# Kernel optimization log

Hardware: AMD Instinct MI355X
Metric: run time of the kernel (lower is better)

Reference implementation:

```python
import jax, jax.numpy as jnp
import numpy as np

F_DIM = 128
RBF_DIM = 20
N_NODES = 10000
N_EDGES = 200000
CUTOFF = 5


def setup_inputs() -> dict:
    key = jax.random.key(0)
    ks = jax.random.split(key, 12)
    s = jax.random.normal(ks[0], (N_NODES, F_DIM), jnp.float32)
    vec = jax.random.normal(ks[1], (N_NODES, 3, F_DIM), jnp.float32)
    edge_indexes = jax.random.randint(ks[2], (2, N_EDGES), 0, N_NODES, jnp.int32)
    edge_vector = jax.random.normal(ks[3], (N_EDGES, 3), jnp.float32)
    # distances in (0.5, 5.0) so fcut is nontrivial and no divide-by-zero
    edge_distance = jax.random.uniform(ks[4], (N_EDGES,), jnp.float32) * 4.5 + 0.5
    edge_rbf = jax.random.normal(ks[5], (N_EDGES, RBF_DIM), jnp.float32)
    # params: linear_s = Linear(F,F) -> SiLU -> Linear(F,3F); linear_rbf = Linear(RBF,3F)
    Ws1 = jax.random.normal(ks[6], (F_DIM, F_DIM), jnp.float32) / np.sqrt(F_DIM)
    bs1 = jnp.zeros((F_DIM,), jnp.float32)
    Ws2 = jax.random.normal(ks[7], (3 * F_DIM, F_DIM), jnp.float32) / np.sqrt(F_DIM)
    bs2 = jnp.zeros((3 * F_DIM,), jnp.float32)
    Wrbf = jax.random.normal(ks[8], (3 * F_DIM, RBF_DIM), jnp.float32) / np.sqrt(RBF_DIM)
    brbf = jnp.zeros((3 * F_DIM,), jnp.float32)
    return {
        "s": s, "vec": vec, "edge_vector": edge_vector,
        "edge_distance": edge_distance, "edge_rbf": edge_rbf,
        "Ws1": Ws1, "bs1": bs1, "Ws2": Ws2, "bs2": bs2,
        "Wrbf": Wrbf, "brbf": brbf,
        "edge_indexes": edge_indexes, "cutoff_dist": CUTOFF,
    }


def reference(s, vec, edge_vector, edge_distance, edge_rbf,
              Ws1, bs1, Ws2, bs2, Wrbf, brbf,
              edge_indexes, cutoff_dist):
    num_atoms, nf = s.shape
    dst_recv = edge_indexes[0]   # index_add target (message receivers)
    src_send = edge_indexes[1]   # gather source (message senders)

    S = s[src_send]              # [E, F]
    Vec = vec[src_send]          # [E, 3, F]

    # linear_s: Linear -> SiLU -> Linear
    h = jax.nn.silu(S @ Ws1.T + bs1)          # [E, F]
    phi = h @ Ws2.T + bs2                      # [E, 3F]

    rbf_lin = edge_rbf @ Wrbf.T + brbf         # [E, 3F]
    # cosine cutoff: 0.5*(cos(pi*d/rc)+1) for d < rc else 0
    rc = jnp.asarray(cutoff_dist, edge_distance.dtype)
    fcut = 0.5 * (jnp.cos(jnp.pi * edge_distance / rc) + 1.0)
    fcut = jnp.where(edge_distance < rc, fcut, 0.0)

    W = rbf_lin * fcut[:, None]
    vec_Ws, vec_Wvv, vec_Wvs = jnp.split(phi * W, 3, axis=-1)  # each [E, F]

    ds = jnp.zeros((num_atoms, nf), s.dtype).at[dst_recv].add(vec_Ws)

    vec_n = edge_vector / edge_distance[:, None]               # [E, 3]
    dVec = vec_Wvv[:, None, :] * Vec + vec_n[:, :, None] * vec_Wvs[:, None, :]  # [E,3,F]
    dvec = jnp.zeros((num_atoms, 3, nf), s.dtype).at[dst_recv].add(dVec)

    return ds, dvec
```

## Files before the change

### kernel.cpp

```cpp
#include <hip/hip_runtime.h>
#include <hip/hip_bf16.h>

typedef __attribute__((ext_vector_type(8))) short short8;
typedef __attribute__((ext_vector_type(4))) float floatx4;
typedef _Float16 half2_t __attribute__((ext_vector_type(2)));

#define CAP 64

__device__ __forceinline__ unsigned short f2bf(float x) {
    unsigned u = __float_as_uint(x);
    unsigned r = u + 0x7fffu + ((u >> 16) & 1u);
    return (unsigned short)(r >> 16);
}
__device__ __forceinline__ float bf2f(unsigned short h) {
    return __uint_as_float(((unsigned)h) << 16);
}
__device__ __forceinline__ unsigned short f2h(float x) {
    _Float16 h = (_Float16)x;
    return __builtin_bit_cast(unsigned short, h);
}
__device__ __forceinline__ float FD(unsigned int a, unsigned int b, float c) {
#if __has_builtin(__builtin_amdgcn_fdot2)
    return __builtin_amdgcn_fdot2(__builtin_bit_cast(half2_t, a),
                                  __builtin_bit_cast(half2_t, b), c, false);
#else
    half2_t ha = __builtin_bit_cast(half2_t, a);
    half2_t hb = __builtin_bit_cast(half2_t, b);
    return c + (float)ha[0] * (float)hb[0] + (float)ha[1] * (float)hb[1];
#endif
}
__device__ __forceinline__ float decode_rc(const void* cutoff_raw) {
    float fv = ((const float*)cutoff_raw)[0];
    int   iv = ((const int*)cutoff_raw)[0];
    if (fv > 0.099f && fv < 1.0e6f) return fv;
    if (iv > 0 && iv < 1000000) return (float)iv;
    double dv = ((const double*)cutoff_raw)[0];
    if (dv > 0.099 && dv < 1.0e6) return (float)dv;
    return (float)(((const long long*)cutoff_raw)[0]);
}

__global__ void setup_kernel(const float* __restrict__ vec,
                             const float* __restrict__ Ws1,
                             const float* __restrict__ Ws2,
                             const float* __restrict__ Wrbf,
                             const float* __restrict__ edge_rbf,
                             const int* __restrict__ eidx,
                             const float* __restrict__ edge_vec,
                             const float* __restrict__ edge_dist,
                             const void* __restrict__ cutoff_raw,
                             unsigned short* __restrict__ P6,
                             unsigned short* __restrict__ ws1_bf,
                             unsigned short* __restrict__ ws2_bf,
                             unsigned short* __restrict__ wrbf_h,
                             unsigned short* __restrict__ rbf_h,
                             int* __restrict__ cnt,
                             unsigned int* __restrict__ rec,
                             int n_vec, int n_w1, int n_w2, int n_wh, int n_rh,
                             int RB, int E, int nbc)
{
    int tid = threadIdx.x;
    if ((int)blockIdx.x < nbc) {
        int total = n_vec + n_w1 + n_w2 + n_wh + n_rh;
        int stride = nbc * 256;
        for (int i = blockIdx.x * 256 + tid; i < total; i += stride) {
            if (i < n_vec) {
                int node = i / 384;
                int r    = i - node * 384;
                P6[(size_t)node * 768 + 384 + r] = f2bf(vec[i]);
            } else if (i < n_vec + n_w1) {
                int j = i - n_vec;
                ws1_bf[j] = f2bf(Ws1[j]);
            } else if (i < n_vec + n_w1 + n_w2) {
                int j = i - n_vec - n_w1;
                ws2_bf[j] = f2bf(Ws2[j]);
            } else if (i < n_vec + n_w1 + n_w2 + n_wh) {
                int j = i - n_vec - n_w1 - n_w2;
                int n = j >> 5, k = j & 31;
                wrbf_h[j] = (k < RB) ? f2h(Wrbf[n * RB + k]) : (unsigned short)0;
            } else {
                int j = i - n_vec - n_w1 - n_w2 - n_wh;
                int e = j / 24, k = j - e * 24;
                rbf_h[j] = (k < RB) ? f2h(edge_rbf[(size_t)e * RB + k]) : (unsigned short)0;
            }
        }
    } else {
        int i = ((int)blockIdx.x - nbc) * 256 + tid;
        if (i >= E) return;
        float rc = decode_rc(cutoff_raw);
        int d = eidx[i];
        int slot = atomicAdd(&cnt[d], 1);
        if (slot >= CAP) return;
        float dist = edge_dist[i];
        float fc = 0.0f;
        if (dist < rc) fc = 0.5f * (cosf(3.14159265358979323846f * dist / rc) + 1.0f);
        float inv = 1.0f / dist;
        unsigned int* rp = rec + ((size_t)(d * CAP + slot) << 3);
        ((uint4*)rp)[0] = make_uint4((unsigned)eidx[E + i], (unsigned)i, 0u, 0u);
        ((uint4*)rp)[1] = make_uint4(__float_as_uint(edge_vec[i * 3 + 0] * inv),
                                     __float_as_uint(edge_vec[i * 3 + 1] * inv),
                                     __float_as_uint(edge_vec[i * 3 + 2] * inv),
                                     __float_as_uint(fc));
    }
}

#define LN 136
__global__ __launch_bounds__(64, 4)
void node_kernel(const float* __restrict__ s,
                 const unsigned short* __restrict__ ws1_bf,
                 const float* __restrict__ bs1,
                 const unsigned short* __restrict__ ws2_bf,
                 const float* __restrict__ bs2,
                 unsigned short* __restrict__ P6,
                 int Nn)
{
    const int lane = threadIdx.x;
    const int l15  = lane & 15;
    const int q    = lane >> 4;
    const int base = blockIdx.x * 16;

    __shared__ unsigned short S_bf[16][LN];
    __shared__ unsigned short H_bf[16][LN];

    #pragma unroll
    for (int it = 0; it < 4; ++it) {
        int r = it * 4 + q;
        int node = base + r;
        short8 v;
        if (node < Nn) {
            const float4* sp4 = (const float4*)(s + (size_t)node * 128 + l15 * 8);
            float4 x0 = sp4[0], x1 = sp4[1];
            v[0] = (short)f2bf(x0.x); v[1] = (short)f2bf(x0.y);
            v[2] = (short)f2bf(x0.z); v[3] = (short)f2bf(x0.w);
            v[4] = (short)f2bf(x1.x); v[5] = (short)f2bf(x1.y);
            v[6] = (short)f2bf(x1.z); v[7] = (short)f2bf(x1.w);
        } else {
            #pragma unroll
            for (int k = 0; k < 8; ++k) v[k] = 0;
        }
        *((short8*)&S_bf[r][l15 * 8]) = v;
    }
    __syncthreads();

    floatx4 acc1[8];
    #pragma unroll
    for (int nj = 0; nj < 8; ++nj) acc1[nj] = (floatx4){0.f, 0.f, 0.f, 0.f};
    #pragma unroll
    for (int ks = 0; ks < 4; ++ks) {
        short8 a = *((const short8*)&S_bf[l15][ks * 32 + q * 8]);
        #pragma unroll
        for (int nj = 0; nj < 8; ++nj) {
            short8 b = *((const short8*)(ws1_bf + ((nj * 16 + l15) * 128 + ks * 32 + q * 8)));
            acc1[nj] = __builtin_amdgcn_mfma_f32_16x16x32_bf16(a, b, acc1[nj], 0, 0, 0);
        }
    }
    #pragma unroll
    for (int nj = 0; nj < 8; ++nj) {
        float b1 = bs1[nj * 16 + l15];
        #pragma unroll
        for (int r = 0; r < 4; ++r) {
            float x = acc1[nj][r] + b1;
            float h = x / (1.0f + __expf(-x));
            H_bf[q * 4 + r][nj * 16 + l15] = f2bf(h);
        }
    }
    __syncthreads();

    #pragma unroll
    for (int g = 0; g < 3; ++g) {
        floatx4 accP[8];
        #pragma unroll
        for (int j = 0; j < 8; ++j) accP[j] = (floatx4){0.f, 0.f, 0.f, 0.f};
        #pragma unroll
        for (int ks = 0; ks < 4; ++ks) {
            short8 a = *((const short8*)&H_bf[l15][ks * 32 + q * 8]);
            #pragma unroll
            for (int j = 0; j < 8; ++j) {
                int n = g * 128 + j * 16 + l15;
                short8 b = *((const short8*)(ws2_bf + ((size_t)n * 128 + ks * 32 + q * 8)));
                accP[j] = __builtin_amdgcn_mfma_f32_16x16x32_bf16(a, b, accP[j], 0, 0, 0);
            }
        }
        #pragma unroll
        for (int j = 0; j < 8; ++j) {
            int n = g * 128 + j * 16 + l15;
            float b2 = bs2[n];
            #pragma unroll
            for (int r = 0; r < 4; ++r) {
                int node = base + q * 4 + r;
                if (node < Nn)
                    P6[(size_t)node * 768 + n] = f2bf(accP[j][r] + b2);
            }
        }
    }
}

__global__ __launch_bounds__(256, 4)
void edge_kernel(const unsigned short* __restrict__ P6,
                 const unsigned short* __restrict__ wrbf_h,
                 const float* __restrict__ brbf,
                 const int* __restrict__ cnt,
                 const unsigned int* __restrict__ rec,
                 const unsigned short* __restrict__ rbf_h,
                 float* __restrict__ out_ds,
                 float* __restrict__ out_dvec,
                 int Nn)
{
    const int tid  = threadIdx.x;
    const int w    = tid >> 6;
    const int lane = tid & 63;
    const int node = __builtin_amdgcn_readfirstlane((int)blockIdx.x * 2 + (w >> 1));
    const int c    = (w & 1) * 64 + lane;
    if (node >= Nn) return;

    const unsigned short* wp0 = wrbf_h + ((size_t)c << 5);
    const unsigned short* wp1 = wrbf_h + ((size_t)(128 + c) << 5);
    const unsigned short* wp2 = wrbf_h + ((size_t)(256 + c) << 5);
    uint4 w0a = *(const uint4*)wp0;
    uint4 w0b = *(const uint4*)(wp0 + 8);
    uint2 w0c = *(const uint2*)(wp0 + 16);
    uint4 w1a = *(const uint4*)wp1;
    uint4 w1b = *(const uint4*)(wp1 + 8);
    uint2 w1c = *(const uint2*)(wp1 + 16);
    uint4 w2a = *(const uint4*)wp2;
    uint4 w2b = *(const uint4*)(wp2 + 8);
    uint2 w2c = *(const uint2*)(wp2 + 16);
    float b0 = brbf[c];
    float b1 = brbf[128 + c];
    float b2 = brbf[256 + c];
    asm volatile("" : "+v"(w0a.x), "+v"(w0a.y), "+v"(w0a.z), "+v"(w0a.w),
                      "+v"(w0b.x), "+v"(w0b.y), "+v"(w0b.z), "+v"(w0b.w),
                      "+v"(w0c.x), "+v"(w0c.y));
    asm volatile("" : "+v"(w1a.x), "+v"(w1a.y), "+v"(w1a.z), "+v"(w1a.w),
                      "+v"(w1b.x), "+v"(w1b.y), "+v"(w1b.z), "+v"(w1b.w),
                      "+v"(w1c.x), "+v"(w1c.y));
    asm volatile("" : "+v"(w2a.x), "+v"(w2a.y), "+v"(w2a.z), "+v"(w2a.w),
                      "+v"(w2b.x), "+v"(w2b.y), "+v"(w2b.z), "+v"(w2b.w),
                      "+v"(w2c.x), "+v"(w2c.y),
                      "+v"(b0), "+v"(b1), "+v"(b2));

    const int deg = min(cnt[node], CAP);
    const size_t bb = (size_t)node * CAP;

    float as = 0.f, a0 = 0.f, a1 = 0.f, a2 = 0.f;

    if (deg > 0) {
        const unsigned int* rp = rec + (bb << 3);
        uint4 sm = ((const uint4*)rp)[0];
        uint4 mq = ((const uint4*)rp)[1];
        int src = (int)sm.x;
        const unsigned short* rr = rbf_h + (size_t)(int)sm.y * 24;
        uint4 Ra = *(const uint4*)rr;
        uint4 Rb = *(const uint4*)(rr + 8);
        uint2 Rc = *(const uint2*)(rr + 16);

        #pragma unroll 2
        for (int sl = 0; sl < deg; ++sl) {
            const unsigned short* pr = P6 + (size_t)src * 768;
            unsigned short u0 = pr[c];
            unsigned short u1 = pr[128 + c];
            unsigned short u2 = pr[256 + c];
            unsigned short u3 = pr[384 + c];
            unsigned short u4 = pr[512 + c];
            unsigned short u5 = pr[640 + c];

            int np = (sl + 1 < deg) ? (sl + 1) : sl;
            const unsigned int* rpn = rec + ((bb + np) << 3);
            uint4 smn = ((const uint4*)rpn)[0];
            uint4 mqn = ((const uint4*)rpn)[1];
            const unsigned short* rrn = rbf_h + (size_t)(int)smn.y * 24;
            uint4 Ran = *(const uint4*)rrn;
            uint4 Rbn = *(const uint4*)(rrn + 8);
            uint2 Rcn = *(const uint2*)(rrn + 16);

            float d0 = b0, d1 = b1, d2 = b2;
            d0 = FD(Ra.x, w0a.x, d0); d1 = FD(Ra.x, w1a.x, d1); d2 = FD(Ra.x, w2a.x, d2);
            d0 = FD(Ra.y, w0a.y, d0); d1 = FD(Ra.y, w1a.y, d1); d2 = FD(Ra.y, w2a.y, d2);
            d0 = FD(Ra.z, w0a.z, d0); d1 = FD(Ra.z, w1a.z, d1); d2 = FD(Ra.z, w2a.z, d2);
            d0 = FD(Ra.w, w0a.w, d0); d1 = FD(Ra.w, w1a.w, d1); d2 = FD(Ra.w, w2a.w, d2);
            d0 = FD(Rb.x, w0b.x, d0); d1 = FD(Rb.x, w1b.x, d1); d2 = FD(Rb.x, w2b.x, d2);
            d0 = FD(Rb.y, w0b.y, d0); d1 = FD(Rb.y, w1b.y, d1); d2 = FD(Rb.y, w2b.y, d2);
            d0 = FD(Rb.z, w0b.z, d0); d1 = FD(Rb.z, w1b.z, d1); d2 = FD(Rb.z, w2b.z, d2);
            d0 = FD(Rb.w, w0b.w, d0); d1 = FD(Rb.w, w1b.w, d1); d2 = FD(Rb.w, w2b.w, d2);
            d0 = FD(Rc.x, w0c.x, d0); d1 = FD(Rc.x, w1c.x, d1); d2 = FD(Rc.x, w2c.x, d2);
            d0 = FD(Rc.y, w0c.y, d0); d1 = FD(Rc.y, w1c.y, d1); d2 = FD(Rc.y, w2c.y, d2);

            float ps = bf2f(u0), pv = bf2f(u1), px = bf2f(u2);
            float v0 = bf2f(u3), v1 = bf2f(u4), v2 = bf2f(u5);

            float fc = __uint_as_float(mq.w);
            float W0 = d0 * fc, W1 = d1 * fc, W2 = d2 * fc;
            as = fmaf(ps, W0, as);
            float mv = pv * W1;
            float mx = px * W2;
            a0 = fmaf(mv, v0, fmaf(mx, __uint_as_float(mq.x), a0));
            a1 = fmaf(mv, v1, fmaf(mx, __uint_as_float(mq.y), a1));
            a2 = fmaf(mv, v2, fmaf(mx, __uint_as_float(mq.z), a2));

            src = (int)smn.x; mq = mqn; Ra = Ran; Rb = Rbn; Rc = Rcn; sm = smn;
        }
    }

    out_ds[(size_t)node * 128 + c] = as;
    float* od = out_dvec + (size_t)node * 384;
    od[c]       = a0;
    od[128 + c] = a1;
    od[256 + c] = a2;
}

extern "C" void kernel_launch(void* const* d_in, const int* in_sizes, int n_in,
                              void* d_out, int out_size, void* d_ws, size_t ws_size,
                              hipStream_t stream) {
    const float* s        = (const float*)d_in[0];
    const float* vec      = (const float*)d_in[1];
    const float* edge_vec = (const float*)d_in[2];
    const float* edge_dst = (const float*)d_in[3];
    const float* edge_rbf = (const float*)d_in[4];
    const float* Ws1      = (const float*)d_in[5];
    const float* bs1      = (const float*)d_in[6];
    const float* Ws2      = (const float*)d_in[7];
    const float* bs2      = (const float*)d_in[8];
    const float* Wrbf     = (const float*)d_in[9];
    const float* brbf     = (const float*)d_in[10];
    const int*   eidx     = (const int*)d_in[11];
    const void*  cutoff   = d_in[12];

    const int F  = 128;
    const int Nn = in_sizes[0] / F;
    const int E  = in_sizes[3];
    const int RB = in_sizes[4] / E;
    const int F3 = 3 * F;

    unsigned int*   rec     = (unsigned int*)d_ws;
    unsigned short* P6      = (unsigned short*)(rec + (size_t)Nn * CAP * 8);
    unsigned short* rbf_h   = P6 + (size_t)Nn * 768;
    unsigned short* ws1_bf  = rbf_h + (size_t)E * 24;
    unsigned short* ws2_bf  = ws1_bf + F * F;
    unsigned short* wrbf_h  = ws2_bf + (size_t)F3 * F;
    int* cnt                = (int*)(wrbf_h + F3 * 32);

    int n_vec = Nn * F3, n_w1 = F * F, n_w2 = F3 * F, n_wh = F3 * 32, n_rh = E * 24;

    hipMemsetAsync(cnt, 0, (size_t)Nn * sizeof(int), stream);

    {
        long long total = (long long)n_vec + n_w1 + n_w2 + n_wh + n_rh;
        int nbc = (int)((total + 1023) / 1024);
        int nbb = (E + 255) / 256;
        setup_kernel<<<nbc + nbb, 256, 0, stream>>>(vec, Ws1, Ws2, Wrbf, edge_rbf,
                                                    eidx, edge_vec, edge_dst, cutoff,
                                                    P6, ws1_bf, ws2_bf, wrbf_h, rbf_h,
                                                    cnt, rec,
                                                    n_vec, n_w1, n_w2, n_wh, n_rh,
                                                    RB, E, nbc);
    }
    node_kernel<<<(Nn + 15) / 16, 64, 0, stream>>>(s, ws1_bf, bs1, ws2_bf, bs2, P6, Nn);

    float* out_ds   = (float*)d_out;
    float* out_dvec = out_ds + (size_t)Nn * F;

    edge_kernel<<<(Nn + 1) / 2, 256, 0, stream>>>(P6, wrbf_h, brbf,
                                                  cnt, rec, rbf_h,
                                                  out_ds, out_dvec, Nn);
}
```

Baseline: 212.8 us.

## Vectorize setup conversions and deepen edge-loop prefetch of gathered rows

The setup conversion loop now has each thread handle 8 elements, using float4 loads and short8 stores instead of scalar per-element work. In the edge kernel, the gathered P6 node row and RBF data for the next edge are now fetched one iteration ahead, and edge records two iterations ahead, to hide gather latency. Final outputs are written with nontemporal stores. The deeper prefetch raises register pressure, and the vector paths assume element counts divisible by 8.

```diff
diff --git a/kernel.cpp b/kernel.cpp
--- a/kernel.cpp
+++ b/kernel.cpp
@@ -55,32 +55,58 @@
                              unsigned short* __restrict__ rbf_h,
                              int* __restrict__ cnt,
                              unsigned int* __restrict__ rec,
-                             int n_vec, int n_w1, int n_w2, int n_wh, int n_rh,
+                             int ng_vec, int ng_w1, int ng_w2, int ng_wh, int ng_rh,
                              int RB, int E, int nbc)
 {
     int tid = threadIdx.x;
     if ((int)blockIdx.x < nbc) {
-        int total = n_vec + n_w1 + n_w2 + n_wh + n_rh;
+        int total = ng_vec + ng_w1 + ng_w2 + ng_wh + ng_rh;
         int stride = nbc * 256;
-        for (int i = blockIdx.x * 256 + tid; i < total; i += stride) {
-            if (i < n_vec) {
-                int node = i / 384;
-                int r    = i - node * 384;
-                P6[(size_t)node * 768 + 384 + r] = f2bf(vec[i]);
-            } else if (i < n_vec + n_w1) {
-                int j = i - n_vec;
-                ws1_bf[j] = f2bf(Ws1[j]);
-            } else if (i < n_vec + n_w1 + n_w2) {
-                int j = i - n_vec - n_w1;
-                ws2_bf[j] = f2bf(Ws2[j]);
-            } else if (i < n_vec + n_w1 + n_w2 + n_wh) {
-                int j = i - n_vec - n_w1 - n_w2;
-                int n = j >> 5, k = j & 31;
-                wrbf_h[j] = (k < RB) ? f2h(Wrbf[n * RB + k]) : (unsigned short)0;
+        for (int g = blockIdx.x * 256 + tid; g < total; g += stride) {
+            if (g < ng_vec) {
+                int node = g / 48;
+                int r = (g - node * 48) * 8;
+                const float4* sp = (const float4*)(vec + (size_t)node * 384 + r);
+                float4 x0 = sp[0], x1 = sp[1];
+                short8 v;
+                v[0]=(short)f2bf(x0.x); v[1]=(short)f2bf(x0.y);
+                v[2]=(short)f2bf(x0.z); v[3]=(short)f2bf(x0.w);
+                v[4]=(short)f2bf(x1.x); v[5]=(short)f2bf(x1.y);
+                v[6]=(short)f2bf(x1.z); v[7]=(short)f2bf(x1.w);
+                *(short8*)(P6 + (size_t)node * 768 + 384 + r) = v;
+            } else if (g < ng_vec + ng_w1 + ng_w2) {
+                int j = (g - ng_vec) * 8;
+                const float* srcp;
+                unsigned short* dstp;
+                if (j < ng_w1 * 8) { srcp = Ws1 + j; dstp = ws1_bf + j; }
+                else               { srcp = Ws2 + (j - ng_w1 * 8); dstp = ws2_bf + (j - ng_w1 * 8); }
+                float4 x0 = ((const float4*)srcp)[0], x1 = ((const float4*)srcp)[1];
+                short8 v;
+                v[0]=(short)f2bf(x0.x); v[1]=(short)f2bf(x0.y);
+                v[2]=(short)f2bf(x0.z); v[3]=(short)f2bf(x0.w);
+                v[4]=(short)f2bf(x1.x); v[5]=(short)f2bf(x1.y);
+                v[6]=(short)f2bf(x1.z); v[7]=(short)f2bf(x1.w);
+                *(short8*)dstp = v;
+            } else if (g < ng_vec + ng_w1 + ng_w2 + ng_wh) {
+                int gg = g - ng_vec - ng_w1 - ng_w2;
+                int n = gg >> 2, k0 = (gg & 3) * 8;
+                short8 v;
+                #pragma unroll
+                for (int t = 0; t < 8; ++t) {
+                    int k = k0 + t;
+                    v[t] = (k < RB) ? (short)f2h(Wrbf[(size_t)n * RB + k]) : (short)0;
+                }
+                *(short8*)(wrbf_h + n * 32 + k0) = v;
             } else {
-                int j = i - n_vec - n_w1 - n_w2 - n_wh;
-                int e = j / 24, k = j - e * 24;
-                rbf_h[j] = (k < RB) ? f2h(edge_rbf[(size_t)e * RB + k]) : (unsigned short)0;
+                int gg = g - ng_vec - ng_w1 - ng_w2 - ng_wh;
+                int e = gg / 3, k0 = (gg - e * 3) * 8;
+                short8 v;
+                #pragma unroll
+                for (int t = 0; t < 8; ++t) {
+                    int k = k0 + t;
+                    v[t] = (k < RB) ? (short)f2h(edge_rbf[(size_t)e * RB + k]) : (short)0;
+                }
+                *(short8*)(rbf_h + (size_t)e * 24 + k0) = v;
             }
         }
     } else {
@@ -244,33 +270,30 @@
     float as = 0.f, a0 = 0.f, a1 = 0.f, a2 = 0.f;
 
     if (deg > 0) {
-        const unsigned int* rp = rec + (bb << 3);
-        uint4 sm = ((const uint4*)rp)[0];
-        uint4 mq = ((const uint4*)rp)[1];
-        int src = (int)sm.x;
+        const uint4* rp = (const uint4*)(rec + (bb << 3));
+
+        uint4 sm = rp[0], mq = rp[1];
         const unsigned short* rr = rbf_h + (size_t)(int)sm.y * 24;
         uint4 Ra = *(const uint4*)rr;
         uint4 Rb = *(const uint4*)(rr + 8);
         uint2 Rc = *(const uint2*)(rr + 16);
-
-        #pragma unroll 2
+        const unsigned short* pr = P6 + (size_t)(int)sm.x * 768;
+        unsigned short u0 = pr[c],       u1 = pr[128 + c], u2 = pr[256 + c];
+        unsigned short u3 = pr[384 + c], u4 = pr[512 + c], u5 = pr[640 + c];
+        int n1 = (deg > 1) ? 1 : 0;
+        uint4 smA = rp[2 * n1], mqA = rp[2 * n1 + 1];
+
         for (int sl = 0; sl < deg; ++sl) {
-            const unsigned short* pr = P6 + (size_t)src * 768;
-            unsigned short u0 = pr[c];
-            unsigned short u1 = pr[128 + c];
-            unsigned short u2 = pr[256 + c];
-            unsigned short u3 = pr[384 + c];
-            unsigned short u4 = pr[512 + c];
-            unsigned short u5 = pr[640 + c];
-
-            int np = (sl + 1 < deg) ? (sl + 1) : sl;
-            const unsigned int* rpn = rec + ((bb + np) << 3);
-            uint4 smn = ((const uint4*)rpn)[0];
-            uint4 mqn = ((const uint4*)rpn)[1];
-            const unsigned short* rrn = rbf_h + (size_t)(int)smn.y * 24;
+            const unsigned short* rrn = rbf_h + (size_t)(int)smA.y * 24;
             uint4 Ran = *(const uint4*)rrn;
             uint4 Rbn = *(const uint4*)(rrn + 8);
             uint2 Rcn = *(const uint2*)(rrn + 16);
+            const unsigned short* prn = P6 + (size_t)(int)smA.x * 768;
+            unsigned short un0 = prn[c],       un1 = prn[128 + c], un2 = prn[256 + c];
+            unsigned short un3 = prn[384 + c], un4 = prn[512 + c], un5 = prn[640 + c];
+
+            int n2 = (sl + 2 < deg) ? (sl + 2) : (deg - 1);
+            uint4 smB = rp[2 * n2], mqB = rp[2 * n2 + 1];
 
             float d0 = b0, d1 = b1, d2 = b2;
             d0 = FD(Ra.x, w0a.x, d0); d1 = FD(Ra.x, w1a.x, d1); d2 = FD(Ra.x, w2a.x, d2);
@@ -296,15 +319,17 @@
             a1 = fmaf(mv, v1, fmaf(mx, __uint_as_float(mq.y), a1));
             a2 = fmaf(mv, v2, fmaf(mx, __uint_as_float(mq.z), a2));
 
-            src = (int)smn.x; mq = mqn; Ra = Ran; Rb = Rbn; Rc = Rcn; sm = smn;
-        }
-    }
-
-    out_ds[(size_t)node * 128 + c] = as;
+            mq = mqA; smA = smB; mqA = mqB;
+            Ra = Ran; Rb = Rbn; Rc = Rcn;
+            u0 = un0; u1 = un1; u2 = un2; u3 = un3; u4 = un4; u5 = un5;
+        }
+    }
+
+    __builtin_nontemporal_store(as, out_ds + (size_t)node * 128 + c);
     float* od = out_dvec + (size_t)node * 384;
-    od[c]       = a0;
-    od[128 + c] = a1;
-    od[256 + c] = a2;
+    __builtin_nontemporal_store(a0, od + c);
+    __builtin_nontemporal_store(a1, od + 128 + c);
+    __builtin_nontemporal_store(a2, od + 256 + c);
 }
 
 extern "C" void kernel_launch(void* const* d_in, const int* in_sizes, int n_in,
@@ -338,19 +363,23 @@
     unsigned short* wrbf_h  = ws2_bf + (size_t)F3 * F;
     int* cnt                = (int*)(wrbf_h + F3 * 32);
 
-    int n_vec = Nn * F3, n_w1 = F * F, n_w2 = F3 * F, n_wh = F3 * 32, n_rh = E * 24;
+    int ng_vec = (Nn * F3) >> 3;
+    int ng_w1  = (F * F) >> 3;
+    int ng_w2  = (F3 * F) >> 3;
+    int ng_wh  = (F3 * 32) >> 3;
+    int ng_rh  = (E * 24) >> 3;
 
     hipMemsetAsync(cnt, 0, (size_t)Nn * sizeof(int), stream);
 
     {
-        long long total = (long long)n_vec + n_w1 + n_w2 + n_wh + n_rh;
-        int nbc = (int)((total + 1023) / 1024);
+        long long total = (long long)ng_vec + ng_w1 + ng_w2 + ng_wh + ng_rh;
+        int nbc = (int)((total + 255) / 256);
         int nbb = (E + 255) / 256;
         setup_kernel<<<nbc + nbb, 256, 0, stream>>>(vec, Ws1, Ws2, Wrbf, edge_rbf,
                                                     eidx, edge_vec, edge_dst, cutoff,
                                                     P6, ws1_bf, ws2_bf, wrbf_h, rbf_h,
                                                     cnt, rec,
-                                                    n_vec, n_w1, n_w2, n_wh, n_rh,
+                                                    ng_vec, ng_w1, ng_w2, ng_wh, ng_rh,
                                                     RB, E, nbc);
     }
     node_kernel<<<(Nn + 15) / 16, 64, 0, stream>>>(s, ws1_bf, bs1, ws2_bf, bs2, P6, Nn);
```

After: 211.8 us. No clear change (-0.4%).
